# Kernel tuning notes

Hardware: AMD Instinct MI355X
Metric: run time of the kernel (lower is better)

## Reference

```python
import jax, jax.numpy as jnp
import numpy as np

N = 50000      # nodes
E = 1600000    # edges per graph
IN = 64
HID = 64
OUT = 64


def _gat_conv(x, edge_index, W, a_src, a_dst, bias):
    """PyG GATConv, heads=1, add_self_loops=True, negative_slope=0.2."""
    n = x.shape[0]
    h = x @ W                                   # [N, d]
    loop = jnp.arange(n, dtype=edge_index.dtype)
    src = jnp.concatenate([edge_index[0], loop])
    dst = jnp.concatenate([edge_index[1], loop])
    e = jax.nn.leaky_relu((h @ a_src)[src] + (h @ a_dst)[dst], negative_slope=0.2)
    m = jax.ops.segment_max(e, dst, num_segments=n)          # stable edge-softmax per dst
    w = jnp.exp(e - m[dst])
    denom = jax.ops.segment_sum(w, dst, num_segments=n)
    alpha = w / denom[dst]                                   # [E+N]
    out = jax.ops.segment_sum(h[src] * alpha[:, None], dst, num_segments=n)
    return out + bias


def setup_inputs() -> dict:
    key = jax.random.key(0)
    ks = jax.random.split(key, 32)

    def glorot(k, shape):
        fan_out = shape[1] if len(shape) > 1 else 1
        lim = (6.0 / (shape[0] + fan_out)) ** 0.5
        return jax.random.uniform(k, shape, minval=-lim, maxval=lim, dtype=jnp.float32)

    inp = {
        "x_ind": jax.random.normal(ks[0], (N, IN), jnp.float32),
        "x_pos": jax.random.normal(ks[1], (N, IN), jnp.float32),
        "edge_ind": jax.random.randint(ks[2], (2, E), 0, N, dtype=jnp.int32),
        "edge_pos": jax.random.randint(ks[3], (2, E), 0, N, dtype=jnp.int32),
        "w1_ind": glorot(ks[4], (IN, HID)),
        "as1_ind": glorot(ks[5], (HID,)),
        "ad1_ind": glorot(ks[6], (HID,)),
        "b1_ind": jnp.zeros((HID,), jnp.float32),
        "w2_ind": glorot(ks[7], (HID, OUT)),
        "as2_ind": glorot(ks[8], (OUT,)),
        "ad2_ind": glorot(ks[9], (OUT,)),
        "b2_ind": jnp.zeros((OUT,), jnp.float32),
        "w1_pos": glorot(ks[10], (IN, HID)),
        "as1_pos": glorot(ks[11], (HID,)),
        "ad1_pos": glorot(ks[12], (HID,)),
        "b1_pos": jnp.zeros((HID,), jnp.float32),
        "w2_pos": glorot(ks[13], (HID, OUT)),
        "as2_pos": glorot(ks[14], (OUT,)),
        "ad2_pos": glorot(ks[15], (OUT,)),
        "b2_pos": jnp.zeros((OUT,), jnp.float32),
        "first_hop_att": glorot(ks[16], (2, HID)),
        "att_weight": glorot(ks[17], (2, OUT)),
        "mlp_w": glorot(ks[18], (OUT, 1)),
        "mlp_b": jnp.zeros((1,), jnp.float32),
    }
    return inp


def reference(x_ind, x_pos, edge_ind, edge_pos,
              w1_ind, as1_ind, ad1_ind, b1_ind,
              w2_ind, as2_ind, ad2_ind, b2_ind,
              w1_pos, as1_pos, ad1_pos, b1_pos,
              w2_pos, as2_pos, ad2_pos, b2_pos,
              first_hop_att, att_weight, mlp_w, mlp_b):
    h_i = jax.nn.relu(_gat_conv(x_ind, edge_ind, w1_ind, as1_ind, ad1_ind, b1_ind))
    h_p = jax.nn.relu(_gat_conv(x_pos, edge_pos, w1_pos, as1_pos, ad1_pos, b1_pos))
    # first-hop branch attention over the two graphs
    s1 = jnp.stack([jnp.sum(first_hop_att[0] * h_i, axis=1),
                    jnp.sum(first_hop_att[1] * h_p, axis=1)], axis=0)  # [2, N]
    a1 = jax.nn.softmax(s1, axis=0)
    fused = a1[0][:, None] * h_i + a1[1][:, None] * h_p
    g_i = _gat_conv(fused, edge_ind, w2_ind, as2_ind, ad2_ind, b2_ind)
    g_p = _gat_conv(fused, edge_pos, w2_pos, as2_pos, ad2_pos, b2_pos)
    s2 = jnp.stack([jnp.sum(att_weight[0] * g_i, axis=1),
                    jnp.sum(att_weight[1] * g_p, axis=1)], axis=0)
    a2 = jax.nn.softmax(s2, axis=0)
    x = a2[0][:, None] * g_i + a2[1][:, None] * g_p
    return x @ mlp_w + mlp_b                    # [N, 1]
```

## Files before the change

### kernel.cpp

```cpp
#include <hip/hip_runtime.h>
#include <hip/hip_fp16.h>

#define ND 64
#define BG 256
#define MAXB 512
#define PCH 16384
#define CAP 9216

__device__ __forceinline__ float lrelu(float x) { return x > 0.f ? x : 0.2f * x; }

__device__ __forceinline__ float wave_sum(float v) {
#pragma unroll
    for (int m = 32; m > 0; m >>= 1) v += __shfl_xor(v, m, 64);
    return v;
}

__device__ __forceinline__ void fma8(float* acc, float w, int4 raw) {
    union { int4 i; __half2 h[4]; } u;
    u.i = raw;
#pragma unroll
    for (int i = 0; i < 4; i++) {
        float2 f = __half22float2(u.h[i]);
        acc[2 * i]     = fmaf(w, f.x, acc[2 * i]);
        acc[2 * i + 1] = fmaf(w, f.y, acc[2 * i + 1]);
    }
}


__global__ void init_cursor(int* __restrict__ bcursor, int nb) {
    int t = threadIdx.x;
    if (t < nb) bcursor[t] = t * CAP;
}

__global__ void partition(const int* __restrict__ eI, const int* __restrict__ eP,
                          int* __restrict__ bcursor, int* __restrict__ part,
                          int N, int E, int nb) {
    __shared__ int hist[MAXB];
    __shared__ int lcur[MAXB];
    int t = threadIdx.x;
    int total = 2 * E;
    int chunkBase = blockIdx.x * PCH;
    int cnt = min(PCH, total - chunkBase);
    int cnt4 = cnt & ~3;
    if (t < nb) hist[t] = 0;
    __syncthreads();
    for (int i = t * 4; i < cnt4; i += 4096) {
        int e = chunkBase + i;
        int4 d; int base;
        if (e + 3 < E)   { d = *(const int4*)(eI + E + e); base = 0; }
        else if (e >= E) { d = *(const int4*)(eP + E + (e - E)); base = N; }
        else {
            int tmp[4];
#pragma unroll
            for (int k = 0; k < 4; k++) {
                int ee = e + k;
                tmp[k] = (ee < E) ? eI[E + ee] : N + eP[E + ee - E];
            }
            d = make_int4(tmp[0], tmp[1], tmp[2], tmp[3]); base = 0;
        }
        atomicAdd(&hist[(base + d.x) >> 8], 1);
        atomicAdd(&hist[(base + d.y) >> 8], 1);
        atomicAdd(&hist[(base + d.z) >> 8], 1);
        atomicAdd(&hist[(base + d.w) >> 8], 1);
    }
    for (int i = cnt4 + t; i < cnt; i += 1024) {
        int e = chunkBase + i;
        int idx = (e < E) ? eI[E + e] : N + eP[E + (e - E)];
        atomicAdd(&hist[idx >> 8], 1);
    }
    __syncthreads();
    if (t < nb) lcur[t] = hist[t] ? atomicAdd(&bcursor[t], hist[t]) : 0;
    __syncthreads();
    for (int i = t * 4; i < cnt4; i += 4096) {
        int e = chunkBase + i;
        int4 s4, d4; int base;
        if (e + 3 < E)   { s4 = *(const int4*)(eI + e); d4 = *(const int4*)(eI + E + e); base = 0; }
        else if (e >= E) { s4 = *(const int4*)(eP + (e - E)); d4 = *(const int4*)(eP + E + (e - E)); base = N; }
        else {
            int ts[4], td[4];
#pragma unroll
            for (int k = 0; k < 4; k++) {
                int ee = e + k;
                if (ee < E) { ts[k] = eI[ee]; td[k] = eI[E + ee]; }
                else        { ts[k] = eP[ee - E]; td[k] = N + eP[E + ee - E]; }
            }
            s4 = make_int4(ts[0], ts[1], ts[2], ts[3]);
            d4 = make_int4(td[0], td[1], td[2], td[3]); base = 0;
        }
        int idx, pos;
        idx = base + d4.x; pos = atomicAdd(&lcur[idx >> 8], 1); part[pos] = (s4.x << 8) | (idx & 255);
        idx = base + d4.y; pos = atomicAdd(&lcur[idx >> 8], 1); part[pos] = (s4.y << 8) | (idx & 255);
        idx = base + d4.z; pos = atomicAdd(&lcur[idx >> 8], 1); part[pos] = (s4.z << 8) | (idx & 255);
        idx = base + d4.w; pos = atomicAdd(&lcur[idx >> 8], 1); part[pos] = (s4.w << 8) | (idx & 255);
    }
    for (int i = cnt4 + t; i < cnt; i += 1024) {
        int e = chunkBase + i;
        int s, idx;
        if (e < E) { s = eI[e]; idx = eI[E + e]; }
        else       { s = eP[e - E]; idx = N + eP[E + (e - E)]; }
        int pos = atomicAdd(&lcur[idx >> 8], 1);
        part[pos] = (s << 8) | (idx & 255);
    }
}

__global__ void bucket_build(const int* __restrict__ part, const int* __restrict__ bcursor,
                             int* __restrict__ row, int* __restrict__ deg,
                             int* __restrict__ csr, int n2) {
    __shared__ int lhist[BG];
    __shared__ int lrow[BG];
    int b = blockIdx.x, t = threadIdx.x;
    int start = b * CAP;
    int cnt = bcursor[b] - start;
    int cnt4 = cnt & ~3;
    if (t < BG) lhist[t] = 0;
    __syncthreads();
    for (int j = t * 4; j < cnt4; j += 4096) {
        int4 p = *(const int4*)(part + start + j);
        atomicAdd(&lhist[p.x & 255], 1);
        atomicAdd(&lhist[p.y & 255], 1);
        atomicAdd(&lhist[p.z & 255], 1);
        atomicAdd(&lhist[p.w & 255], 1);
    }
    for (int j = cnt4 + t; j < cnt; j += 1024) atomicAdd(&lhist[part[start + j] & 255], 1);
    __syncthreads();
    int v = 0;
    if (t < BG) { v = lhist[t]; lrow[t] = v; }
    __syncthreads();
    for (int off = 1; off < BG; off <<= 1) {
        int a = (t < BG && t >= off) ? lrow[t - off] : 0;
        __syncthreads();
        if (t < BG) lrow[t] += a;
        __syncthreads();
    }
    if (t < BG) {
        int excl = lrow[t] - v;
        int g = b * BG + t;
        if (g < n2) { row[g] = start + excl; deg[g] = v; }
        lhist[t] = start + excl;
    }
    __syncthreads();
    for (int j = t * 4; j < cnt4; j += 4096) {
        int4 p = *(const int4*)(part + start + j);
        int pos;
        pos = atomicAdd(&lhist[p.x & 255], 1); csr[pos] = p.x >> 8;
        pos = atomicAdd(&lhist[p.y & 255], 1); csr[pos] = p.y >> 8;
        pos = atomicAdd(&lhist[p.z & 255], 1); csr[pos] = p.z >> 8;
        pos = atomicAdd(&lhist[p.w & 255], 1); csr[pos] = p.w >> 8;
    }
    for (int j = cnt4 + t; j < cnt; j += 1024) {
        int p = part[start + j];
        int pos = atomicAdd(&lhist[p & 255], 1);
        csr[pos] = p >> 8;
    }
}

__global__ void gemm_dual(const float* __restrict__ xA, const float* __restrict__ xB,
                          const float* __restrict__ WA, const float* __restrict__ WB,
                          const float* __restrict__ asA, const float* __restrict__ adA,
                          const float* __restrict__ asB, const float* __restrict__ adB,
                          __half* __restrict__ h16, float* __restrict__ ssrc,
                          float* __restrict__ sdst, int N) {
    int half = blockIdx.x & 1;
    int blk = blockIdx.x >> 1;
    int wave = threadIdx.x >> 6;
    int lane = threadIdx.x & 63;
    const float* x  = half ? xB : xA;
    const float* W  = half ? WB : WA;
    const float* av_ = half ? asB : asA;
    const float* dv_ = half ? adB : adA;
    int nodeBase = (blk * 4 + wave) * 4;
    __shared__ float xs[4][4 * ND];

    if (nodeBase + 3 < N) {
        *(float4*)&xs[wave][lane * 4] = *(const float4*)&x[(size_t)nodeBase * ND + lane * 4];
    } else if (nodeBase < N) {
#pragma unroll
        for (int i = 0; i < 4; i++) {
            int gi = nodeBase * ND + lane * 4 + i;
            xs[wave][lane * 4 + i] = (gi < N * ND) ? x[gi] : 0.f;
        }
    }
    __syncthreads();
    if (nodeBase >= N) return;

    float4 acc = {0.f, 0.f, 0.f, 0.f};
#pragma unroll
    for (int k = 0; k < ND; k++) {
        float wv = W[k * ND + lane];
        acc.x = fmaf(xs[wave][0 * ND + k], wv, acc.x);
        acc.y = fmaf(xs[wave][1 * ND + k], wv, acc.y);
        acc.z = fmaf(xs[wave][2 * ND + k], wv, acc.z);
        acc.w = fmaf(xs[wave][3 * ND + k], wv, acc.w);
    }
    float av = av_[lane], dv = dv_[lane];
    float s1x = wave_sum(acc.x * av), s2x = wave_sum(acc.x * dv);
    float s1y = wave_sum(acc.y * av), s2y = wave_sum(acc.y * dv);
    float s1z = wave_sum(acc.z * av), s2z = wave_sum(acc.z * dv);
    float s1w = wave_sum(acc.w * av), s2w = wave_sum(acc.w * dv);

    int g0 = half * N + nodeBase;
    h16[(size_t)(g0 + 0) * ND + lane] = __float2half(acc.x);
    if (nodeBase + 1 < N) h16[(size_t)(g0 + 1) * ND + lane] = __float2half(acc.y);
    if (nodeBase + 2 < N) h16[(size_t)(g0 + 2) * ND + lane] = __float2half(acc.z);
    if (nodeBase + 3 < N) h16[(size_t)(g0 + 3) * ND + lane] = __float2half(acc.w);
    if (lane == 0) {
        ssrc[g0] = s1x; sdst[g0] = s2x;
        if (nodeBase + 1 < N) { ssrc[g0 + 1] = s1y; sdst[g0 + 1] = s2y; }
        if (nodeBase + 2 < N) { ssrc[g0 + 2] = s1z; sdst[g0 + 2] = s2z; }
        if (nodeBase + 3 < N) { ssrc[g0 + 3] = s1w; sdst[g0 + 3] = s2w; }
    }
}

__global__ void aggregate_dual(const int* __restrict__ csr, const int* __restrict__ row,
                               const int* __restrict__ deg, const float* __restrict__ ssrc,
                               const float* __restrict__ sdst, const __half* __restrict__ h16,
                               const float* __restrict__ bA, const float* __restrict__ bB,
                               float* __restrict__ out, int N, int relu) {
    int half = blockIdx.x & 1;
    int wave = threadIdx.x >> 6;
    int lane = threadIdx.x & 63;
    int sub  = lane >> 4;
    int l16  = lane & 15;
    int slot = l16 >> 3;
    int fl8  = (l16 & 7) * 8;
    int node = ((blockIdx.x >> 1) * 4 + wave) * 4 + sub;
    bool valid = node < N;
    int g = half * N + node;
    const float* bias = half ? bB : bA;
    const float* ss = ssrc + (size_t)half * N;
    const __half* hh = h16 + (size_t)half * N * ND;

    int start = valid ? row[g] : 0;
    int cnt   = valid ? deg[g] : 0;
    float sd  = valid ? sdst[g] : 0.f;
    float wself = valid ? __expf(lrelu(ss[node] + sd)) : 0.f;

    float acc[8] = {0.f, 0.f, 0.f, 0.f, 0.f, 0.f, 0.f, 0.f};
    float denomp = 0.f;
    int waveBase = sub << 4;

    for (int base = 0; base < cnt; base += 16) {
        int c16 = min(16, cnt - base);
        int sj = (l16 < c16) ? csr[start + base + l16] : 0;
        float wj = (l16 < c16) ? __expf(lrelu(ss[sj] + sd)) : 0.f;
        denomp += wj;
        int nq = (c16 + 1) >> 1;
        float w0 = __shfl(wj, waveBase + slot, 64);
        int s0 = __shfl(sj, waveBase + slot, 64);
        int4 raw0 = *(const int4*)(hh + (size_t)s0 * ND + fl8);
        for (int c = 1; c < nq; c++) {
            float w1 = __shfl(wj, waveBase + c * 2 + slot, 64);
            int s1 = __shfl(sj, waveBase + c * 2 + slot, 64);
            int4 raw1 = *(const int4*)(hh + (size_t)s1 * ND + fl8);
            fma8(acc, w0, raw0);
            w0 = w1; raw0 = raw1;
        }
        fma8(acc, w0, raw0);
    }

#pragma unroll
    for (int i = 0; i < 8; i++) acc[i] += __shfl_xor(acc[i], 8, 64);
#pragma unroll
    for (int m = 1; m <= 8; m <<= 1) denomp += __shfl_xor(denomp, m, 64);
    float denom = denomp + wself;

    if (!valid || slot != 0) return;
    int4 rawS = *(const int4*)(hh + (size_t)node * ND + fl8);
    union { int4 i; __half2 h[4]; } us;
    us.i = rawS;
    float v[8];
#pragma unroll
    for (int i = 0; i < 4; i++) {
        float2 f = __half22float2(us.h[i]);
        v[2 * i]     = (acc[2 * i]     + wself * f.x) / denom + bias[fl8 + 2 * i];
        v[2 * i + 1] = (acc[2 * i + 1] + wself * f.y) / denom + bias[fl8 + 2 * i + 1];
    }
    if (relu) {
#pragma unroll
        for (int i = 0; i < 8; i++) v[i] = fmaxf(v[i], 0.f);
    }
    *(float4*)&out[(size_t)g * ND + fl8]     = make_float4(v[0], v[1], v[2], v[3]);
    *(float4*)&out[(size_t)g * ND + fl8 + 4] = make_float4(v[4], v[5], v[6], v[7]);
}

__global__ void branch_att(const float* __restrict__ hbig, const float* __restrict__ att,
                           float* __restrict__ fused, int n) {
    int gid = blockIdx.x * blockDim.x + threadIdx.x;
    int node = gid >> 6, lane = gid & 63;
    if (node >= n) return;
    float vi = hbig[(size_t)node * ND + lane];
    float vp = hbig[((size_t)n + node) * ND + lane];
    float s0 = wave_sum(att[lane] * vi);
    float s1 = wave_sum(att[ND + lane] * vp);
    float m = fmaxf(s0, s1);
    float a0 = __expf(s0 - m), a1 = __expf(s1 - m);
    fused[(size_t)node * ND + lane] = (a0 * vi + a1 * vp) / (a0 + a1);
}

__global__ void branch_att_mlp(const float* __restrict__ hbig, const float* __restrict__ att,
                               const float* __restrict__ mlpw, const float* __restrict__ mlpb,
                               float* __restrict__ out, int n) {
    int gid = blockIdx.x * blockDim.x + threadIdx.x;
    int node = gid >> 6, lane = gid & 63;
    if (node >= n) return;
    float vi = hbig[(size_t)node * ND + lane];
    float vp = hbig[((size_t)n + node) * ND + lane];
    float s0 = wave_sum(att[lane] * vi);
    float s1 = wave_sum(att[ND + lane] * vp);
    float m = fmaxf(s0, s1);
    float a0 = __expf(s0 - m), a1 = __expf(s1 - m);
    float xj = (a0 * vi + a1 * vp) / (a0 + a1);
    float o = wave_sum(xj * mlpw[lane]);
    if (lane == 0) out[node] = o + mlpb[0];
}

extern "C" void kernel_launch(void* const* d_in, const int* in_sizes, int n_in,
                              void* d_out, int out_size, void* d_ws, size_t ws_size,
                              hipStream_t stream) {
    const int N = in_sizes[0] / ND;
    const int E = in_sizes[2] / 2;

    const float* x_ind = (const float*)d_in[0];
    const float* x_pos = (const float*)d_in[1];
    const int*   e_ind = (const int*)d_in[2];
    const int*   e_pos = (const int*)d_in[3];
    const float* w1i = (const float*)d_in[4];
    const float* as1i = (const float*)d_in[5];
    const float* ad1i = (const float*)d_in[6];
    const float* b1i = (const float*)d_in[7];
    const float* w2i = (const float*)d_in[8];
    const float* as2i = (const float*)d_in[9];
    const float* ad2i = (const float*)d_in[10];
    const float* b2i = (const float*)d_in[11];
    const float* w1p = (const float*)d_in[12];
    const float* as1p = (const float*)d_in[13];
    const float* ad1p = (const float*)d_in[14];
    const float* b1p = (const float*)d_in[15];
    const float* w2p = (const float*)d_in[16];
    const float* as2p = (const float*)d_in[17];
    const float* ad2p = (const float*)d_in[18];
    const float* b2p = (const float*)d_in[19];
    const float* fha = (const float*)d_in[20];
    const float* attw = (const float*)d_in[21];
    const float* mlpw = (const float*)d_in[22];
    const float* mlpb = (const float*)d_in[23];

    char* ws = (char*)d_ws;
    size_t off = 0;
    auto alloc = [&](size_t elems) { void* p = ws + off; off += elems * 4; return p; };

    const int n2 = 2 * N;
    const int nb = (n2 + BG - 1) / BG;

    __half* h16 = (__half*)alloc((size_t)n2 * ND / 2);
    float* hbig = (float*)alloc((size_t)n2 * ND);
    float* bufC = (float*)alloc((size_t)N * ND);
    float* ssrc = (float*)alloc(n2);
    float* sdst = (float*)alloc(n2);
    int* deg    = (int*)alloc(n2);
    int* rowi   = (int*)alloc(n2);
    int* csr    = (int*)alloc((size_t)nb * CAP);
    int* bcursor= (int*)alloc(MAXB);
    int* part   = (int*)hbig;

    const int gemmBlocks = 2 * ((N + 15) / 16);
    const int aggBlocks  = 2 * ((N + 15) / 16);
    const int nodeBlocks = (N + 3) / 4;
    const int partBlocks = (2 * E + PCH - 1) / PCH;

    init_cursor<<<1, 512, 0, stream>>>(bcursor, nb);
    partition<<<partBlocks, 1024, 0, stream>>>(e_ind, e_pos, bcursor, part, N, E, nb);
    bucket_build<<<nb, 1024, 0, stream>>>(part, bcursor, rowi, deg, csr, n2);

    gemm_dual<<<gemmBlocks, 256, 0, stream>>>(x_ind, x_pos, w1i, w1p,
                                              as1i, ad1i, as1p, ad1p,
                                              h16, ssrc, sdst, N);
    aggregate_dual<<<aggBlocks, 256, 0, stream>>>(csr, rowi, deg, ssrc, sdst, h16,
                                                  b1i, b1p, hbig, N, 1);
    branch_att<<<nodeBlocks, 256, 0, stream>>>(hbig, fha, bufC, N);

    gemm_dual<<<gemmBlocks, 256, 0, stream>>>(bufC, bufC, w2i, w2p,
                                              as2i, ad2i, as2p, ad2p,
                                              h16, ssrc, sdst, N);
    aggregate_dual<<<aggBlocks, 256, 0, stream>>>(csr, rowi, deg, ssrc, sdst, h16,
                                                  b2i, b2p, hbig, N, 0);
    branch_att_mlp<<<nodeBlocks, 256, 0, stream>>>(hbig, attw, mlpw, mlpb,
                                                   (float*)d_out, N);
}
```

Measured before the change: 351.7 us.

## Fuse edge partitioning with first-layer GEMM into one launch; deepen aggregate prefetch

```diff
diff --git a/kernel.cpp b/kernel.cpp
--- a/kernel.cpp
+++ b/kernel.cpp
@@ -32,11 +32,10 @@
     if (t < nb) bcursor[t] = t * CAP;
 }
 
-__global__ void partition(const int* __restrict__ eI, const int* __restrict__ eP,
-                          int* __restrict__ bcursor, int* __restrict__ part,
-                          int N, int E, int nb) {
-    __shared__ int hist[MAXB];
-    __shared__ int lcur[MAXB];
+__device__ void partition_body(int* hist, int* lcur,
+                               const int* __restrict__ eI, const int* __restrict__ eP,
+                               int* __restrict__ bcursor, int* __restrict__ part,
+                               int N, int E, int nb) {
     int t = threadIdx.x;
     int total = 2 * E;
     int chunkBase = blockIdx.x * PCH;
@@ -103,6 +102,82 @@
     }
 }
 
+__device__ void gemm_body(float* xsAll, int gb,
+                          const float* __restrict__ xA, const float* __restrict__ xB,
+                          const float* __restrict__ WA, const float* __restrict__ WB,
+                          const float* __restrict__ asA, const float* __restrict__ adA,
+                          const float* __restrict__ asB, const float* __restrict__ adB,
+                          __half* __restrict__ h16, float* __restrict__ ssrc,
+                          float* __restrict__ sdst, int N) {
+    int half = gb & 1;
+    int blk = gb >> 1;
+    int wave = threadIdx.x >> 6;
+    int lane = threadIdx.x & 63;
+    const float* x  = half ? xB : xA;
+    const float* W  = half ? WB : WA;
+    const float* av_ = half ? asB : asA;
+    const float* dv_ = half ? adB : adA;
+    int nodeBase = (blk * 16 + wave) * 4;
+    float* xs = xsAll + wave * (4 * ND);
+
+    if (nodeBase + 3 < N) {
+        *(float4*)&xs[lane * 4] = *(const float4*)&x[(size_t)nodeBase * ND + lane * 4];
+    } else if (nodeBase < N) {
+#pragma unroll
+        for (int i = 0; i < 4; i++) {
+            int gi = nodeBase * ND + lane * 4 + i;
+            xs[lane * 4 + i] = (gi < N * ND) ? x[gi] : 0.f;
+        }
+    }
+    __syncthreads();
+    if (nodeBase >= N) return;
+
+    float4 acc = {0.f, 0.f, 0.f, 0.f};
+#pragma unroll
+    for (int k = 0; k < ND; k++) {
+        float wv = W[k * ND + lane];
+        acc.x = fmaf(xs[0 * ND + k], wv, acc.x);
+        acc.y = fmaf(xs[1 * ND + k], wv, acc.y);
+        acc.z = fmaf(xs[2 * ND + k], wv, acc.z);
+        acc.w = fmaf(xs[3 * ND + k], wv, acc.w);
+    }
+    float av = av_[lane], dv = dv_[lane];
+    float s1x = wave_sum(acc.x * av), s2x = wave_sum(acc.x * dv);
+    float s1y = wave_sum(acc.y * av), s2y = wave_sum(acc.y * dv);
+    float s1z = wave_sum(acc.z * av), s2z = wave_sum(acc.z * dv);
+    float s1w = wave_sum(acc.w * av), s2w = wave_sum(acc.w * dv);
+
+    int g0 = half * N + nodeBase;
+    h16[(size_t)(g0 + 0) * ND + lane] = __float2half(acc.x);
+    if (nodeBase + 1 < N) h16[(size_t)(g0 + 1) * ND + lane] = __float2half(acc.y);
+    if (nodeBase + 2 < N) h16[(size_t)(g0 + 2) * ND + lane] = __float2half(acc.z);
+    if (nodeBase + 3 < N) h16[(size_t)(g0 + 3) * ND + lane] = __float2half(acc.w);
+    if (lane == 0) {
+        ssrc[g0] = s1x; sdst[g0] = s2x;
+        if (nodeBase + 1 < N) { ssrc[g0 + 1] = s1y; sdst[g0 + 1] = s2y; }
+        if (nodeBase + 2 < N) { ssrc[g0 + 2] = s1z; sdst[g0 + 2] = s2z; }
+        if (nodeBase + 3 < N) { ssrc[g0 + 3] = s1w; sdst[g0 + 3] = s2w; }
+    }
+}
+
+__global__ void __launch_bounds__(1024) part_gemm(
+        const int* __restrict__ eI, const int* __restrict__ eP,
+        int* __restrict__ bcursor, int* __restrict__ part,
+        const float* __restrict__ xA, const float* __restrict__ xB,
+        const float* __restrict__ WA, const float* __restrict__ WB,
+        const float* __restrict__ asA, const float* __restrict__ adA,
+        const float* __restrict__ asB, const float* __restrict__ adB,
+        __half* __restrict__ h16, float* __restrict__ ssrc, float* __restrict__ sdst,
+        int N, int E, int nb, int partBlocks) {
+    __shared__ int smem[16 * 4 * ND];
+    if (blockIdx.x < partBlocks) {
+        partition_body(smem, smem + MAXB, eI, eP, bcursor, part, N, E, nb);
+    } else {
+        gemm_body((float*)smem, blockIdx.x - partBlocks,
+                  xA, xB, WA, WB, asA, adA, asB, adB, h16, ssrc, sdst, N);
+    }
+}
+
 __global__ void bucket_build(const int* __restrict__ part, const int* __restrict__ bcursor,
                              int* __restrict__ row, int* __restrict__ deg,
                              int* __restrict__ csr, int n2) {
@@ -160,44 +235,42 @@
                           const float* __restrict__ asB, const float* __restrict__ adB,
                           __half* __restrict__ h16, float* __restrict__ ssrc,
                           float* __restrict__ sdst, int N) {
+    __shared__ float xs[16][4 * ND];
+    int wave = threadIdx.x >> 6;
     int half = blockIdx.x & 1;
     int blk = blockIdx.x >> 1;
-    int wave = threadIdx.x >> 6;
     int lane = threadIdx.x & 63;
     const float* x  = half ? xB : xA;
     const float* W  = half ? WB : WA;
     const float* av_ = half ? asB : asA;
     const float* dv_ = half ? adB : adA;
     int nodeBase = (blk * 4 + wave) * 4;
-    __shared__ float xs[4][4 * ND];
-
+    float* xsw = xs[wave];
     if (nodeBase + 3 < N) {
-        *(float4*)&xs[wave][lane * 4] = *(const float4*)&x[(size_t)nodeBase * ND + lane * 4];
+        *(float4*)&xsw[lane * 4] = *(const float4*)&x[(size_t)nodeBase * ND + lane * 4];
     } else if (nodeBase < N) {
 #pragma unroll
         for (int i = 0; i < 4; i++) {
             int gi = nodeBase * ND + lane * 4 + i;
-            xs[wave][lane * 4 + i] = (gi < N * ND) ? x[gi] : 0.f;
+            xsw[lane * 4 + i] = (gi < N * ND) ? x[gi] : 0.f;
         }
     }
     __syncthreads();
     if (nodeBase >= N) return;
-
     float4 acc = {0.f, 0.f, 0.f, 0.f};
 #pragma unroll
     for (int k = 0; k < ND; k++) {
         float wv = W[k * ND + lane];
-        acc.x = fmaf(xs[wave][0 * ND + k], wv, acc.x);
-        acc.y = fmaf(xs[wave][1 * ND + k], wv, acc.y);
-        acc.z = fmaf(xs[wave][2 * ND + k], wv, acc.z);
-        acc.w = fmaf(xs[wave][3 * ND + k], wv, acc.w);
+        acc.x = fmaf(xsw[0 * ND + k], wv, acc.x);
+        acc.y = fmaf(xsw[1 * ND + k], wv, acc.y);
+        acc.z = fmaf(xsw[2 * ND + k], wv, acc.z);
+        acc.w = fmaf(xsw[3 * ND + k], wv, acc.w);
     }
     float av = av_[lane], dv = dv_[lane];
     float s1x = wave_sum(acc.x * av), s2x = wave_sum(acc.x * dv);
     float s1y = wave_sum(acc.y * av), s2y = wave_sum(acc.y * dv);
     float s1z = wave_sum(acc.z * av), s2z = wave_sum(acc.z * dv);
     float s1w = wave_sum(acc.w * av), s2w = wave_sum(acc.w * dv);
-
     int g0 = half * N + nodeBase;
     h16[(size_t)(g0 + 0) * ND + lane] = __float2half(acc.x);
     if (nodeBase + 1 < N) h16[(size_t)(g0 + 1) * ND + lane] = __float2half(acc.y);
@@ -247,15 +320,21 @@
         int nq = (c16 + 1) >> 1;
         float w0 = __shfl(wj, waveBase + slot, 64);
         int s0 = __shfl(sj, waveBase + slot, 64);
-        int4 raw0 = *(const int4*)(hh + (size_t)s0 * ND + fl8);
-        for (int c = 1; c < nq; c++) {
-            float w1 = __shfl(wj, waveBase + c * 2 + slot, 64);
-            int s1 = __shfl(sj, waveBase + c * 2 + slot, 64);
-            int4 raw1 = *(const int4*)(hh + (size_t)s1 * ND + fl8);
-            fma8(acc, w0, raw0);
-            w0 = w1; raw0 = raw1;
+        int4 r0 = *(const int4*)(hh + (size_t)s0 * ND + fl8);
+        if (nq == 1) { fma8(acc, w0, r0); continue; }
+        float w1 = __shfl(wj, waveBase + 2 + slot, 64);
+        int s1 = __shfl(sj, waveBase + 2 + slot, 64);
+        int4 r1 = *(const int4*)(hh + (size_t)s1 * ND + fl8);
+        for (int c = 2; c < nq; c++) {
+            float w2 = __shfl(wj, waveBase + c * 2 + slot, 64);
+            int s2 = __shfl(sj, waveBase + c * 2 + slot, 64);
+            int4 r2 = *(const int4*)(hh + (size_t)s2 * ND + fl8);
+            fma8(acc, w0, r0);
+            w0 = w1; r0 = r1;
+            w1 = w2; r1 = r2;
         }
-        fma8(acc, w0, raw0);
+        fma8(acc, w0, r0);
+        fma8(acc, w1, r1);
     }
 
 #pragma unroll
@@ -363,25 +442,26 @@
     int* bcursor= (int*)alloc(MAXB);
     int* part   = (int*)hbig;
 
-    const int gemmBlocks = 2 * ((N + 15) / 16);
-    const int aggBlocks  = 2 * ((N + 15) / 16);
-    const int nodeBlocks = (N + 3) / 4;
-    const int partBlocks = (2 * E + PCH - 1) / PCH;
+    const int partBlocks  = (2 * E + PCH - 1) / PCH;
+    const int gemm1Blocks = 2 * ((N + 63) / 64);
+    const int gemm2Blocks = 2 * ((N + 15) / 16);
+    const int aggBlocks   = 2 * ((N + 15) / 16);
+    const int nodeBlocks  = (N + 3) / 4;
 
     init_cursor<<<1, 512, 0, stream>>>(bcursor, nb);
-    partition<<<partBlocks, 1024, 0, stream>>>(e_ind, e_pos, bcursor, part, N, E, nb);
+    part_gemm<<<partBlocks + gemm1Blocks, 1024, 0, stream>>>(
+        e_ind, e_pos, bcursor, part,
+        x_ind, x_pos, w1i, w1p, as1i, ad1i, as1p, ad1p,
+        h16, ssrc, sdst, N, E, nb, partBlocks);
     bucket_build<<<nb, 1024, 0, stream>>>(part, bcursor, rowi, deg, csr, n2);
 
-    gemm_dual<<<gemmBlocks, 256, 0, stream>>>(x_ind, x_pos, w1i, w1p,
-                                              as1i, ad1i, as1p, ad1p,
-                                              h16, ssrc, sdst, N);
     aggregate_dual<<<aggBlocks, 256, 0, stream>>>(csr, rowi, deg, ssrc, sdst, h16,
                                                   b1i, b1p, hbig, N, 1);
     branch_att<<<nodeBlocks, 256, 0, stream>>>(hbig, fha, bufC, N);
 
-    gemm_dual<<<gemmBlocks, 256, 0, stream>>>(bufC, bufC, w2i, w2p,
-                                              as2i, ad2i, as2p, ad2p,
-                                              h16, ssrc, sdst, N);
+    gemm_dual<<<gemm2Blocks, 256, 0, stream>>>(bufC, bufC, w2i, w2p,
+                                               as2i, ad2i, as2p, ad2p,
+                                               h16, ssrc, sdst, N);
     aggregate_dual<<<aggBlocks, 256, 0, stream>>>(csr, rowi, deg, ssrc, sdst, h16,
                                                   b2i, b2p, hbig, N, 0);
     branch_att_mlp<<<nodeBlocks, 256, 0, stream>>>(hbig, attw, mlpw, mlpb,
```

New measurement: 342.1 us. -2.7%, faster.
